# Performance work log

Hardware: AMD Instinct MI355X
Metric: run time of the kernel (lower is better)

The kernel has to match this reference:

```python
import jax, jax.numpy as jnp
import numpy as np

H = 4096        # hidden_size
NH = 32         # heads
HD = H // NH    # head_dim = 128
EPS = 1e-5
MINUS_INF = -10000.0
B, S = 2, 1024


def setup_inputs() -> dict:
    key = jax.random.key(0)
    ks = jax.random.split(key, 7)
    x = jax.random.normal(ks[0], (B, S, H), jnp.float32)
    mask = jnp.zeros((B, 1, 1, S), jnp.float32)  # additive padding mask (0 = keep)
    norm_w = 1.0 + 0.02 * jax.random.normal(ks[1], (H,), jnp.float32)
    norm_b = 0.02 * jax.random.normal(ks[2], (H,), jnp.float32)
    qkv_w = 0.02 * jax.random.normal(ks[3], (H, 3 * H), jnp.float32)
    qkv_b = 0.02 * jax.random.normal(ks[4], (3 * H,), jnp.float32)
    attn_ow = 0.02 * jax.random.normal(ks[5], (H, H), jnp.float32)
    return {"x": x, "mask": mask, "norm_w": norm_w, "norm_b": norm_b,
            "qkv_w": qkv_w, "qkv_b": qkv_b, "attn_ow": attn_ow}


def reference(x, mask, norm_w, norm_b, qkv_w, qkv_b, attn_ow):
    b, s, h = x.shape
    # --- pre-attention layernorm (qkv_gemm fuses this in DeepSpeed) ---
    mu = jnp.mean(x, axis=-1, keepdims=True)
    var = jnp.mean(jnp.square(x - mu), axis=-1, keepdims=True)
    inp_norm = (x - mu) * jax.lax.rsqrt(var + EPS) * norm_w + norm_b
    # --- fused QKV GEMM + bias ---
    qkv = inp_norm @ qkv_w + qkv_b                      # [b, s, 3H]
    q, k, v = jnp.split(qkv, 3, axis=-1)
    q = q.reshape(b, s, NH, HD).transpose(0, 2, 1, 3)   # [b, nh, s, hd]
    k = k.reshape(b, s, NH, HD).transpose(0, 2, 1, 3)
    v = v.reshape(b, s, NH, HD).transpose(0, 2, 1, 3)
    # --- scaled dot-product with triangular (causal) mask + additive input mask ---
    norm_factor = 1.0 / jnp.sqrt(jnp.asarray(HD, x.dtype))
    scores = jnp.einsum('bhqd,bhkd->bhqk', q, k) * norm_factor  # [b, nh, s, s]
    causal = jnp.where(jnp.tril(jnp.ones((s, s), bool)), 0.0, MINUS_INF).astype(x.dtype)
    probs = jax.nn.softmax(scores + causal + mask, axis=-1)
    ctx = jnp.einsum('bhqk,bhkd->bhqd', probs, v)               # [b, nh, s, hd]
    ctx = ctx.transpose(0, 2, 1, 3).reshape(b, s, h)
    # --- output projection (vector_matmul, bias applied later in MLP residual-add) ---
    out = ctx @ attn_ow
    return out
```

## Files before the change

### kernel.cpp

```cpp
#include <hip/hip_runtime.h>
#include <stdint.h>


#define S_LEN 1024
#define HID   4096
#define NHEAD 32
#define HDIM  128

typedef __attribute__((ext_vector_type(8))) short bf16x8;
typedef __attribute__((ext_vector_type(4))) float f32x4;
typedef __attribute__((ext_vector_type(8))) unsigned short us8;

__device__ __forceinline__ unsigned short f2bf(float f) {
    union { float f; unsigned u; } v; v.f = f;
    unsigned r = v.u + 0x7fffu + ((v.u >> 16) & 1u);
    return (unsigned short)(r >> 16);
}

__device__ __forceinline__ void gld16(const unsigned short* g, unsigned short* l) {
    __builtin_amdgcn_global_load_lds(
        (const __attribute__((address_space(1))) void*)g,
        (__attribute__((address_space(3))) void*)l, 16, 0, 0);
}

__global__ __launch_bounds__(256) void ln_kernel(const float* __restrict__ x,
        const float* __restrict__ w, const float* __restrict__ bch,
        unsigned short* __restrict__ out) {
    const int row = blockIdx.x;
    const int t = threadIdx.x;
    const float* xr = x + (size_t)row * HID;
    float4 v[4];
    float sum = 0.f, sq = 0.f;
#pragma unroll
    for (int i = 0; i < 4; i++) {
        v[i] = ((const float4*)xr)[t + (i << 8)];
        sum += v[i].x + v[i].y + v[i].z + v[i].w;
        sq  += v[i].x*v[i].x + v[i].y*v[i].y + v[i].z*v[i].z + v[i].w*v[i].w;
    }
#pragma unroll
    for (int off = 32; off; off >>= 1) {
        sum += __shfl_down(sum, off);
        sq  += __shfl_down(sq, off);
    }
    __shared__ float ssum[4], ssq[4];
    if ((t & 63) == 0) { ssum[t >> 6] = sum; ssq[t >> 6] = sq; }
    __syncthreads();
    const float s_all = ssum[0] + ssum[1] + ssum[2] + ssum[3];
    const float q_all = ssq[0] + ssq[1] + ssq[2] + ssq[3];
    const float mean = s_all * (1.f / HID);
    const float var  = q_all * (1.f / HID) - mean * mean;
    const float rstd = rsqrtf(var + 1e-5f);
    unsigned short* orow = out + (size_t)row * HID;
#pragma unroll
    for (int i = 0; i < 4; i++) {
        float4 wv = ((const float4*)w)[t + (i << 8)];
        float4 bv = ((const float4*)bch)[t + (i << 8)];
        ushort4 o;
        o.x = f2bf((v[i].x - mean) * rstd * wv.x + bv.x);
        o.y = f2bf((v[i].y - mean) * rstd * wv.y + bv.y);
        o.z = f2bf((v[i].z - mean) * rstd * wv.z + bv.z);
        o.w = f2bf((v[i].w - mean) * rstd * wv.w + bv.w);
        ((ushort4*)orow)[t + (i << 8)] = o;
    }
}

__global__ __launch_bounds__(256) void transconv(const float* __restrict__ W,
        unsigned short* __restrict__ Wt, int K, int N) {
    __shared__ float tileT[128 * 65];
    const int n0 = blockIdx.x << 7, k0 = blockIdx.y << 6;
    const int t = threadIdx.x;
#pragma unroll
    for (int it = 0; it < 8; it++) {
        int idx = (it << 8) + t;
        int r = idx >> 5;
        int c4 = idx & 31;
        float4 v = *(const float4*)(W + (size_t)(k0 + r) * N + n0 + (c4 << 2));
        tileT[((c4 << 2) + 0) * 65 + r] = v.x;
        tileT[((c4 << 2) + 1) * 65 + r] = v.y;
        tileT[((c4 << 2) + 2) * 65 + r] = v.z;
        tileT[((c4 << 2) + 3) * 65 + r] = v.w;
    }
    __syncthreads();
#pragma unroll
    for (int it = 0; it < 4; it++) {
        int idx = (it << 8) + t;
        int n = idx >> 3;
        int k8 = idx & 7;
        const float* src = &tileT[n * 65 + (k8 << 3)];
        us8 o;
#pragma unroll
        for (int e = 0; e < 8; e++) o[e] = f2bf(src[e]);
        *(us8*)(Wt + (size_t)(n0 + n) * K + k0 + (k8 << 3)) = o;
    }
}


#define T256_PHASE(CB, KS, IH, READ_B, STAGE_CALL, DO_VM)                         \
  {                                                                               \
    _Pragma("unroll") for (int ii = 0; ii < 4; ii++)                              \
        af[ii] = ldA(CB, KS, ((IH) << 2) + ii);                                   \
    if (READ_B) {                                                                 \
      _Pragma("unroll") for (int jj = 0; jj < 4; jj++) bfv[jj] = ldB(CB, KS, jj); \
    }                                                                             \
    STAGE_CALL;                                                                   \
    __builtin_amdgcn_s_barrier();                                                 \
    asm volatile("s_waitcnt lgkmcnt(0)" ::: "memory");                            \
    __builtin_amdgcn_sched_barrier(0);                                            \
    __builtin_amdgcn_s_setprio(1);                                                \
    _Pragma("unroll") for (int ii = 0; ii < 4; ii++)                              \
      _Pragma("unroll") for (int jj = 0; jj < 4; jj++)                            \
        acc[((IH) << 2) + ii][jj] = __builtin_amdgcn_mfma_f32_16x16x32_bf16(      \
            af[ii], bfv[jj], acc[((IH) << 2) + ii][jj], 0, 0, 0);                 \
    __builtin_amdgcn_s_setprio(0);                                                \
    if (DO_VM) asm volatile("s_waitcnt vmcnt(4)" ::: "memory");                   \
    __builtin_amdgcn_s_barrier();                                                 \
  }

#define T256_TILE(TT, CB, PT)                                                     \
  {                                                                               \
    bf16x8 af[4], bfv[4];                                                         \
    T256_PHASE(CB, 0, 0, 1, stage(GA, (((CB)^1) << 15)        , (PT), 0), 0)      \
    T256_PHASE(CB, 0, 1, 0, stage(GB, (((CB)^1) << 15) + 16384, (PT), 0), 1)      \
    T256_PHASE(CB, 1, 0, 1, stage(GA, (((CB)^1) << 15) +  8192, (PT), 1), 0)      \
    T256_PHASE(CB, 1, 1, 0, stage(GB, (((CB)^1) << 15) + 24576, (PT), 1), 1)      \
  }

__device__ __forceinline__ void gemm_core_256(
        const unsigned short* __restrict__ GA,
        const unsigned short* __restrict__ GB,
        unsigned short* lds,
        f32x4 acc[8][4]) {
    const int t = threadIdx.x;
    const int wave = t >> 6, lane = t & 63, quad = lane >> 4, l16 = lane & 15;
    const int waveM = wave >> 2, waveN = wave & 3;
    const int sq8 = (((lane & 3) ^ ((lane >> 3) & 3)) << 3);

    auto stage = [&](const unsigned short* G, int ldsOff, int tau, int ks) {
#pragma unroll
        for (int u = 0; u < 2; u++) {
            const int grp = (u << 3) + wave;
            const int r = (grp << 4) + (lane >> 2);
            gld16(G + ((size_t)r << 12) + (tau << 6) + (ks << 5) + sq8,
                  lds + ldsOff + (grp << 9));
        }
    };
    auto ldA = [&](int buf, int ks, int i) -> bf16x8 {
        const int r = (waveM << 7) + (i << 4) + l16;
        return ((const bf16x8*)(lds + (buf << 15) + (ks << 13)))
            [(r << 2) + (quad ^ ((r >> 1) & 3))];
    };
    auto ldB = [&](int buf, int ks, int j) -> bf16x8 {
        const int r = (waveN << 6) + (j << 4) + l16;
        return ((const bf16x8*)(lds + (buf << 15) + 16384 + (ks << 13)))
            [(r << 2) + (quad ^ ((r >> 1) & 3))];
    };

    stage(GA, 0,     0, 0);
    stage(GB, 16384, 0, 0);
    stage(GA, 8192,  0, 1);
    stage(GB, 24576, 0, 1);
    asm volatile("s_waitcnt vmcnt(4)" ::: "memory");
    __builtin_amdgcn_s_barrier();

    for (int tt = 0; tt < 64; tt += 2) {
        T256_TILE(tt,     0, tt + 1)
        T256_TILE(tt + 1, 1, (tt == 62) ? 63 : tt + 2)
    }
    asm volatile("s_waitcnt vmcnt(0)" ::: "memory");
}

__global__ __launch_bounds__(512, 2) void gemm_qkv16(
        const unsigned short* __restrict__ A,
        const unsigned short* __restrict__ Bt,
        const float* __restrict__ bias,
        unsigned short* __restrict__ qb,
        unsigned short* __restrict__ kb,
        unsigned short* __restrict__ vt) {
    __shared__ unsigned short lds[65536];
    const int orig = blockIdx.x;
    const int bm = orig & 7, bn = orig >> 3;
    const int t = threadIdx.x;
    const int wave = t >> 6, lane = t & 63, quad = lane >> 4, l16 = lane & 15;
    const int waveM = wave >> 2, waveN = wave & 3;

    const f32x4 fz = {0.f, 0.f, 0.f, 0.f};
    f32x4 acc[8][4];
#pragma unroll
    for (int i = 0; i < 8; i++)
#pragma unroll
        for (int j = 0; j < 4; j++) acc[i][j] = fz;

    gemm_core_256(A + ((size_t)bm << 20), Bt + ((size_t)bn << 20), lds, acc);

    const int nbase = (bn << 8) + (waveN << 6);
    const int which = nbase >> 12;
#pragma unroll
    for (int ii = 0; ii < 8; ii++) {
#pragma unroll
        for (int jj = 0; jj < 4; jj++) {
#pragma unroll
            for (int r = 0; r < 4; r++) {
                int m = (bm << 8) + (waveM << 7) + (ii << 4) + (quad << 2) + r;
                int n = nbase + (jj << 4) + l16;
                float v = acc[ii][jj][r] + bias[n];
                unsigned short bvv = f2bf(v);
                int bb = m >> 10, s = m & 1023;
                int h = n & 4095, head = h >> 7, hd = h & 127;
                size_t bh = (size_t)(bb << 5) + head;
                if (which == 0)      qb[(bh * S_LEN + s) * HDIM + hd] = bvv;
                else if (which == 1) kb[(bh * S_LEN + s) * HDIM + hd] = bvv;
                else                 vt[(bh * HDIM + hd) * S_LEN + s] = bvv;
            }
        }
    }
}


#define GEMM_PHASE(CB, KS, PFT, PFB, DO_VM)                                       \
  {                                                                               \
    bf16x8 af[4], bfv[4];                                                         \
    _Pragma("unroll") for (int ii = 0; ii < 4; ii++) af[ii] = ldA(CB, KS, ii);    \
    _Pragma("unroll") for (int jj = 0; jj < 4; jj++) bfv[jj] = ldB(CB, KS, jj);   \
    stageA(PFT, KS, PFB);                                                         \
    stageB(PFT, KS, PFB);                                                         \
    __builtin_amdgcn_s_barrier();                                                 \
    asm volatile("s_waitcnt lgkmcnt(0)" ::: "memory");                            \
    __builtin_amdgcn_sched_barrier(0);                                            \
    __builtin_amdgcn_s_setprio(1);                                                \
    _Pragma("unroll") for (int ii = 0; ii < 4; ii++)                              \
      _Pragma("unroll") for (int jj = 0; jj < 4; jj++)                            \
        acc[ii][jj] = __builtin_amdgcn_mfma_f32_16x16x32_bf16(                    \
            af[ii], bfv[jj], acc[ii][jj], 0, 0, 0);                               \
    __builtin_amdgcn_s_setprio(0);                                                \
    if (DO_VM) asm volatile("s_waitcnt vmcnt(6)" ::: "memory");                   \
    __builtin_amdgcn_s_barrier();                                                 \
  }

#define GEMM_TILE(TT, CB)                                                         \
  {                                                                               \
    int pf_ = (TT) + 2; if (pf_ > 63) pf_ = 63;                                   \
    GEMM_PHASE(CB, 0, pf_, ((CB) + 2) % 3, 0)                                     \
    GEMM_PHASE(CB, 1, pf_, ((CB) + 2) % 3, 1)                                     \
  }

__device__ __forceinline__ void gemm_core_8w(
        const unsigned short* __restrict__ GA,
        const unsigned short* __restrict__ GB,
        unsigned short* lds,
        f32x4 acc[4][4]) {
    const int t = threadIdx.x;
    const int wave = t >> 6, lane = t & 63, quad = lane >> 4, l16 = lane & 15;
    const int waveM = wave >> 2, waveN = wave & 3;
    const int srow = lane >> 2;
    const int scol = (((lane & 3) ^ ((lane >> 3) & 3)) << 3);

    auto stageA = [&](int tau, int ks, int buf) {
        const int row = (wave << 4) + srow;
        gld16(GA + ((size_t)row << 12) + (tau << 6) + (ks << 5) + scol,
              lds + buf * 24576 + (ks << 12) + (wave << 9));
    };
    auto stageB = [&](int tau, int ks, int buf) {
#pragma unroll
        for (int u = 0; u < 2; u++) {
            const int ii = (wave << 1) + u;
            const int row = (ii << 4) + srow;
            gld16(GB + ((size_t)row << 12) + (tau << 6) + (ks << 5) + scol,
                  lds + buf * 24576 + 8192 + (ks << 13) + (ii << 9));
        }
    };
    auto ldA = [&](int buf, int ks, int ii) -> bf16x8 {
        const int r = (waveM << 6) + (ii << 4) + l16;
        return ((const bf16x8*)(lds + buf * 24576 + (ks << 12)))
            [(r << 2) + (quad ^ ((r >> 1) & 3))];
    };
    auto ldB = [&](int buf, int ks, int jj) -> bf16x8 {
        const int r = (waveN << 6) + (jj << 4) + l16;
        return ((const bf16x8*)(lds + buf * 24576 + 8192 + (ks << 13)))
            [(r << 2) + (quad ^ ((r >> 1) & 3))];
    };

    stageA(0, 0, 0); stageB(0, 0, 0); stageA(0, 1, 0); stageB(0, 1, 0);
    stageA(1, 0, 1); stageB(1, 0, 1); stageA(1, 1, 1); stageB(1, 1, 1);
    asm volatile("s_waitcnt vmcnt(6)" ::: "memory");
    __builtin_amdgcn_s_barrier();

    for (int tb = 0; tb < 63; tb += 3) {
        GEMM_TILE(tb,     0)
        GEMM_TILE(tb + 1, 1)
        GEMM_TILE(tb + 2, 2)
    }
    GEMM_TILE(63, 0)
    asm volatile("s_waitcnt vmcnt(0)" ::: "memory");
}

__global__ __launch_bounds__(512, 2) void gemm_proj8(
        const unsigned short* __restrict__ A,
        const unsigned short* __restrict__ Bt,
        float* __restrict__ outf) {
    __shared__ unsigned short lds[73728];
    const int orig = blockIdx.x;
    const int wg = ((orig & 7) * 32) + (orig >> 3);
    const int bm = wg >> 4, bn = wg & 15;
    const int t = threadIdx.x;
    const int wave = t >> 6, lane = t & 63, quad = lane >> 4, l16 = lane & 15;
    const int waveM = wave >> 2, waveN = wave & 3;

    const f32x4 fz = {0.f, 0.f, 0.f, 0.f};
    f32x4 acc[4][4];
#pragma unroll
    for (int i = 0; i < 4; i++)
#pragma unroll
        for (int j = 0; j < 4; j++) acc[i][j] = fz;

    gemm_core_8w(A + ((size_t)bm << 19), Bt + ((size_t)bn << 20), lds, acc);

#pragma unroll
    for (int ii = 0; ii < 4; ii++)
#pragma unroll
        for (int jj = 0; jj < 4; jj++)
#pragma unroll
            for (int r = 0; r < 4; r++) {
                int m = (bm << 7) + (waveM << 6) + (ii << 4) + (quad << 2) + r;
                int n = (bn << 8) + (waveN << 6) + (jj << 4) + l16;
                outf[((size_t)m << 12) + n] = acc[ii][jj][r];
            }
}

__global__ __launch_bounds__(256) void attn_kernel(
        const unsigned short* __restrict__ qbuf,
        const unsigned short* __restrict__ kbuf,
        const unsigned short* __restrict__ vtbuf,
        const float* __restrict__ mask,
        unsigned short* __restrict__ ctx) {
    __shared__ unsigned short q_lds[64 * 128];
    __shared__ unsigned short k_lds[64 * 128];
    __shared__ unsigned short v_lds[128 * 64];
    __shared__ unsigned short p_lds[64 * 64];
    const int t = threadIdx.x;
    const int wave = t >> 6, lane = t & 63, quad = lane >> 4, l16 = lane & 15;
    const int bq = blockIdx.x, bh = blockIdx.y;
    const int q0 = bq << 6;
    const int b = bh >> 5;
    const unsigned short* Q  = qbuf  + (size_t)bh * S_LEN * HDIM;
    const unsigned short* Kp = kbuf  + (size_t)bh * S_LEN * HDIM;
    const unsigned short* Vp = vtbuf + (size_t)bh * HDIM * S_LEN;

    {
        int r = t >> 4, c = (t & 15) << 3;
#pragma unroll
        for (int it = 0; it < 4; it++)
            gld16(Q + (size_t)(q0 + r + (it << 4)) * HDIM + c,
                  q_lds + ((((it << 8) + (wave << 6))) << 3));
    }

    const f32x4 fz = {0.f, 0.f, 0.f, 0.f};
    f32x4 o[8];
#pragma unroll
    for (int n = 0; n < 8; n++) o[n] = fz;
    float l_i[4] = {0.f, 0.f, 0.f, 0.f};
    const float scale = 0.08838834764831845f;
    const float* mrow = mask + b * S_LEN;

    for (int kt = 0; kt <= bq; kt++) {
        const int k0 = kt << 6;
        {
            int rk = t >> 4, ck = (t & 15) << 3;
            int rv = t >> 3, cv = (t & 7) << 3;
#pragma unroll
            for (int it = 0; it < 4; it++) {
                gld16(Kp + (size_t)(k0 + rk + (it << 4)) * HDIM + ck,
                      k_lds + (((it << 8) + (wave << 6)) << 3));
                gld16(Vp + (size_t)(rv + (it << 5)) * S_LEN + k0 + cv,
                      v_lds + (((it << 8) + (wave << 6)) << 3));
            }
        }
        __syncthreads();

        f32x4 sacc[4];
#pragma unroll
        for (int j = 0; j < 4; j++) sacc[j] = fz;
        const bf16x8* qv = (const bf16x8*)q_lds;
        const bf16x8* kv = (const bf16x8*)k_lds;
#pragma unroll
        for (int kk = 0; kk < 4; kk++) {
            bf16x8 aq = qv[(((wave << 4) + l16) << 4) + (kk << 2) + quad];
#pragma unroll
            for (int j = 0; j < 4; j++) {
                bf16x8 bk = kv[((((j << 4) + l16)) << 4) + (kk << 2) + quad];
                sacc[j] = __builtin_amdgcn_mfma_f32_16x16x32_bf16(aq, bk, sacc[j], 0, 0, 0);
            }
        }

#pragma unroll
        for (int r = 0; r < 4; r++) {
            int qrow = q0 + (wave << 4) + (quad << 2) + r;
#pragma unroll
            for (int j = 0; j < 4; j++) {
                int key = k0 + (j << 4) + l16;
                float x = sacc[j][r] * scale + mrow[key];
                if (key > qrow) x -= 10000.0f;
                float p = __expf(x);
                l_i[r] += p;
                p_lds[((wave << 4) + (quad << 2) + r) * 64 + (j << 4) + l16] = f2bf(p);
            }
        }
        __syncthreads();

        const bf16x8* pvv = (const bf16x8*)p_lds;
        const bf16x8* vv = (const bf16x8*)v_lds;
#pragma unroll
        for (int ks = 0; ks < 2; ks++) {
            bf16x8 ap = pvv[(((wave << 4) + l16) << 3) + (ks << 2) + quad];
#pragma unroll
            for (int n = 0; n < 8; n++) {
                bf16x8 bvv = vv[((((n << 4) + l16)) << 3) + (ks << 2) + quad];
                o[n] = __builtin_amdgcn_mfma_f32_16x16x32_bf16(ap, bvv, o[n], 0, 0, 0);
            }
        }
        __syncthreads();
    }

#pragma unroll
    for (int r = 0; r < 4; r++) {
        float l = l_i[r];
#pragma unroll
        for (int off = 1; off < 16; off <<= 1) l += __shfl_xor(l, off);
        float inv = 1.0f / l;
        int qrow = q0 + (wave << 4) + (quad << 2) + r;
        size_t base = ((size_t)(b * S_LEN + qrow)) * HID + ((size_t)(bh & 31) << 7);
#pragma unroll
        for (int n = 0; n < 8; n++)
            ctx[base + (n << 4) + l16] = f2bf(o[n][r] * inv);
    }
}

extern "C" void kernel_launch(void* const* d_in, const int* in_sizes, int n_in,
                              void* d_out, int out_size, void* d_ws, size_t ws_size,
                              hipStream_t stream) {
    const float* x       = (const float*)d_in[0];
    const float* mask    = (const float*)d_in[1];
    const float* norm_w  = (const float*)d_in[2];
    const float* norm_b  = (const float*)d_in[3];
    const float* qkv_w   = (const float*)d_in[4];
    const float* qkv_b   = (const float*)d_in[5];
    const float* attn_ow = (const float*)d_in[6];
    float* out = (float*)d_out;

    char* ws = (char*)d_ws;
    size_t off = 0;
    auto alloc = [&](size_t bytes) {
        char* p = ws + off;
        off += (bytes + 255) & ~(size_t)255;
        return p;
    };
    unsigned short* inp_norm = (unsigned short*)alloc((size_t)2048 * HID * 2);
    unsigned short* qkv_wt   = (unsigned short*)alloc((size_t)3 * HID * HID * 2);
    unsigned short* ow_t     = (unsigned short*)alloc((size_t)HID * HID * 2);
    unsigned short* qb       = (unsigned short*)alloc((size_t)64 * S_LEN * HDIM * 2);
    unsigned short* kb       = (unsigned short*)alloc((size_t)64 * S_LEN * HDIM * 2);
    unsigned short* vt       = (unsigned short*)alloc((size_t)64 * S_LEN * HDIM * 2);
    unsigned short* ctx      = (unsigned short*)alloc((size_t)2048 * HID * 2);

    ln_kernel<<<2048, 256, 0, stream>>>(x, norm_w, norm_b, inp_norm);
    transconv<<<dim3(3 * HID / 128, HID / 64), 256, 0, stream>>>(qkv_w, qkv_wt, HID, 3 * HID);
    transconv<<<dim3(HID / 128, HID / 64), 256, 0, stream>>>(attn_ow, ow_t, HID, HID);
    gemm_qkv16<<<384, 512, 0, stream>>>(inp_norm, qkv_wt, qkv_b, qb, kb, vt);
    attn_kernel<<<dim3(16, 64), 256, 0, stream>>>(qb, kb, vt, mask, ctx);
    gemm_proj8<<<256, 512, 0, stream>>>(ctx, ow_t, out);
}
```

Before: 810.5 us.

## Retile QKV GEMM to 256x192 blocks for full wave occupancy across CUs

The QKV GEMM moves from 256x256 output tiles (384 blocks) to 256x192 tiles (512 blocks). Each wave now computes 8x3 MFMA tiles, and the B tile is staged once per K-step with a new 8-way swizzle. The goal is to fix wave quantization on the 256-CU part (384 blocks leaves a partial second wave at 2 blocks per CU) and to cut LDS use. The projection GEMM's prefetch staging is also regrouped into its first phase. In exchange, arithmetic intensity per block drops, since the B:A reuse ratio is lower.

```diff
diff --git a/kernel.cpp b/kernel.cpp
--- a/kernel.cpp
+++ b/kernel.cpp
@@ -95,116 +95,117 @@
 }
 
 
-#define T256_PHASE(CB, KS, IH, READ_B, STAGE_CALL, DO_VM)                         \
+#define Q_PHASE(CB, KS, IH, READB, STAGE, VMSTMT)                                 \
   {                                                                               \
     _Pragma("unroll") for (int ii = 0; ii < 4; ii++)                              \
         af[ii] = ldA(CB, KS, ((IH) << 2) + ii);                                   \
-    if (READ_B) {                                                                 \
-      _Pragma("unroll") for (int jj = 0; jj < 4; jj++) bfv[jj] = ldB(CB, KS, jj); \
+    if (READB) {                                                                  \
+      _Pragma("unroll") for (int jj = 0; jj < 3; jj++) bfv[jj] = ldB(CB, KS, jj); \
     }                                                                             \
-    STAGE_CALL;                                                                   \
+    STAGE;                                                                        \
     __builtin_amdgcn_s_barrier();                                                 \
     asm volatile("s_waitcnt lgkmcnt(0)" ::: "memory");                            \
     __builtin_amdgcn_sched_barrier(0);                                            \
     __builtin_amdgcn_s_setprio(1);                                                \
     _Pragma("unroll") for (int ii = 0; ii < 4; ii++)                              \
-      _Pragma("unroll") for (int jj = 0; jj < 4; jj++)                            \
+      _Pragma("unroll") for (int jj = 0; jj < 3; jj++)                            \
         acc[((IH) << 2) + ii][jj] = __builtin_amdgcn_mfma_f32_16x16x32_bf16(      \
             af[ii], bfv[jj], acc[((IH) << 2) + ii][jj], 0, 0, 0);                 \
     __builtin_amdgcn_s_setprio(0);                                                \
-    if (DO_VM) asm volatile("s_waitcnt vmcnt(4)" ::: "memory");                   \
+    VMSTMT;                                                                       \
     __builtin_amdgcn_s_barrier();                                                 \
   }
 
-#define T256_TILE(TT, CB, PT)                                                     \
+#define Q_TILE(TT, CB)                                                            \
   {                                                                               \
-    bf16x8 af[4], bfv[4];                                                         \
-    T256_PHASE(CB, 0, 0, 1, stage(GA, (((CB)^1) << 15)        , (PT), 0), 0)      \
-    T256_PHASE(CB, 0, 1, 0, stage(GB, (((CB)^1) << 15) + 16384, (PT), 0), 1)      \
-    T256_PHASE(CB, 1, 0, 1, stage(GA, (((CB)^1) << 15) +  8192, (PT), 1), 0)      \
-    T256_PHASE(CB, 1, 1, 0, stage(GB, (((CB)^1) << 15) + 24576, (PT), 1), 1)      \
+    bf16x8 af[4], bfv[3];                                                         \
+    int pf_ = (TT) + 1; if (pf_ > 63) pf_ = 63;                                   \
+    Q_PHASE(CB, 0, 0, 1, { stgA(pf_, 0, (CB)^1); stgB(pf_, (CB)^1); }, ((void)0)) \
+    Q_PHASE(CB, 0, 1, 0, ((void)0), asm volatile("s_waitcnt vmcnt(5)":::"memory"))\
+    Q_PHASE(CB, 1, 0, 1, { stgA(pf_, 1, (CB)^1); }, ((void)0))                    \
+    Q_PHASE(CB, 1, 1, 0, ((void)0), asm volatile("s_waitcnt vmcnt(2)":::"memory"))\
   }
 
-__device__ __forceinline__ void gemm_core_256(
-        const unsigned short* __restrict__ GA,
-        const unsigned short* __restrict__ GB,
-        unsigned short* lds,
-        f32x4 acc[8][4]) {
-    const int t = threadIdx.x;
-    const int wave = t >> 6, lane = t & 63, quad = lane >> 4, l16 = lane & 15;
-    const int waveM = wave >> 2, waveN = wave & 3;
-    const int sq8 = (((lane & 3) ^ ((lane >> 3) & 3)) << 3);
-
-    auto stage = [&](const unsigned short* G, int ldsOff, int tau, int ks) {
-#pragma unroll
-        for (int u = 0; u < 2; u++) {
-            const int grp = (u << 3) + wave;
-            const int r = (grp << 4) + (lane >> 2);
-            gld16(G + ((size_t)r << 12) + (tau << 6) + (ks << 5) + sq8,
-                  lds + ldsOff + (grp << 9));
-        }
-    };
-    auto ldA = [&](int buf, int ks, int i) -> bf16x8 {
-        const int r = (waveM << 7) + (i << 4) + l16;
-        return ((const bf16x8*)(lds + (buf << 15) + (ks << 13)))
-            [(r << 2) + (quad ^ ((r >> 1) & 3))];
-    };
-    auto ldB = [&](int buf, int ks, int j) -> bf16x8 {
-        const int r = (waveN << 6) + (j << 4) + l16;
-        return ((const bf16x8*)(lds + (buf << 15) + 16384 + (ks << 13)))
-            [(r << 2) + (quad ^ ((r >> 1) & 3))];
-    };
-
-    stage(GA, 0,     0, 0);
-    stage(GB, 16384, 0, 0);
-    stage(GA, 8192,  0, 1);
-    stage(GB, 24576, 0, 1);
-    asm volatile("s_waitcnt vmcnt(4)" ::: "memory");
-    __builtin_amdgcn_s_barrier();
-
-    for (int tt = 0; tt < 64; tt += 2) {
-        T256_TILE(tt,     0, tt + 1)
-        T256_TILE(tt + 1, 1, (tt == 62) ? 63 : tt + 2)
-    }
-    asm volatile("s_waitcnt vmcnt(0)" ::: "memory");
-}
-
-__global__ __launch_bounds__(512, 2) void gemm_qkv16(
+__global__ __launch_bounds__(512, 2) void gemm_qkv192(
         const unsigned short* __restrict__ A,
         const unsigned short* __restrict__ Bt,
         const float* __restrict__ bias,
         unsigned short* __restrict__ qb,
         unsigned short* __restrict__ kb,
         unsigned short* __restrict__ vt) {
-    __shared__ unsigned short lds[65536];
+    __shared__ unsigned short lds[57344];
     const int orig = blockIdx.x;
     const int bm = orig & 7, bn = orig >> 3;
     const int t = threadIdx.x;
     const int wave = t >> 6, lane = t & 63, quad = lane >> 4, l16 = lane & 15;
     const int waveM = wave >> 2, waveN = wave & 3;
 
+    const unsigned short* GA = A  + ((size_t)bm << 8) * HID;
+    const unsigned short* GB = Bt + ((size_t)bn * 192) * HID;
+
+    const int sqa = (((lane & 3) ^ ((lane >> 3) & 3)) << 3);
+    const int sqb = (((lane & 7) ^ ((lane >> 3) & 7)) << 3);
+
+    auto stgA = [&](int tau, int ks, int buf) {
+#pragma unroll
+        for (int u = 0; u < 2; u++) {
+            const int g = (u << 3) + wave;
+            const int row = (g << 4) + (lane >> 2);
+            gld16(GA + (size_t)row * HID + (tau << 6) + (ks << 5) + sqa,
+                  lds + buf * 28672 + (ks << 13) + (g << 9));
+        }
+    };
+    auto stgB = [&](int tau, int buf) {
+#pragma unroll
+        for (int u = 0; u < 3; u++) {
+            const int g = (u << 3) + wave;
+            const int row = (g << 3) + (lane >> 3);
+            gld16(GB + (size_t)row * HID + (tau << 6) + sqb,
+                  lds + buf * 28672 + 16384 + (g << 9));
+        }
+    };
+    auto ldA = [&](int buf, int ks, int i) -> bf16x8 {
+        const int r = (waveM << 7) + (i << 4) + l16;
+        return ((const bf16x8*)lds)
+            [((buf * 28672 + (ks << 13)) >> 3) + (r << 2) + (quad ^ ((r >> 1) & 3))];
+    };
+    auto ldB = [&](int buf, int ks, int j) -> bf16x8 {
+        const int r = waveN * 48 + (j << 4) + l16;
+        return ((const bf16x8*)lds)
+            [((buf * 28672 + 16384) >> 3) + (r << 3) + (((ks << 2) | quad) ^ (r & 7))];
+    };
+
     const f32x4 fz = {0.f, 0.f, 0.f, 0.f};
-    f32x4 acc[8][4];
+    f32x4 acc[8][3];
 #pragma unroll
     for (int i = 0; i < 8; i++)
 #pragma unroll
-        for (int j = 0; j < 4; j++) acc[i][j] = fz;
-
-    gemm_core_256(A + ((size_t)bm << 20), Bt + ((size_t)bn << 20), lds, acc);
-
-    const int nbase = (bn << 8) + (waveN << 6);
-    const int which = nbase >> 12;
+        for (int j = 0; j < 3; j++) acc[i][j] = fz;
+
+    stgA(0, 0, 0);
+    stgB(0, 0);
+    stgA(0, 1, 0);
+    asm volatile("s_waitcnt vmcnt(2)" ::: "memory");
+    __builtin_amdgcn_s_barrier();
+
+    for (int tt = 0; tt < 64; tt += 2) {
+        Q_TILE(tt,     0)
+        Q_TILE(tt + 1, 1)
+    }
+    asm volatile("s_waitcnt vmcnt(0)" ::: "memory");
+
 #pragma unroll
     for (int ii = 0; ii < 8; ii++) {
 #pragma unroll
-        for (int jj = 0; jj < 4; jj++) {
+        for (int jj = 0; jj < 3; jj++) {
 #pragma unroll
             for (int r = 0; r < 4; r++) {
                 int m = (bm << 8) + (waveM << 7) + (ii << 4) + (quad << 2) + r;
-                int n = nbase + (jj << 4) + l16;
+                int n = bn * 192 + waveN * 48 + (jj << 4) + l16;
                 float v = acc[ii][jj][r] + bias[n];
                 unsigned short bvv = f2bf(v);
                 int bb = m >> 10, s = m & 1023;
+                int which = n >> 12;
                 int h = n & 4095, head = h >> 7, hd = h & 127;
                 size_t bh = (size_t)(bb << 5) + head;
                 if (which == 0)      qb[(bh * S_LEN + s) * HDIM + hd] = bvv;
@@ -216,13 +217,12 @@
 }
 
 
-#define GEMM_PHASE(CB, KS, PFT, PFB, DO_VM)                                       \
+#define GEMM_PHASE(CB, KS, STAGE, VMSTMT)                                         \
   {                                                                               \
     bf16x8 af[4], bfv[4];                                                         \
     _Pragma("unroll") for (int ii = 0; ii < 4; ii++) af[ii] = ldA(CB, KS, ii);    \
     _Pragma("unroll") for (int jj = 0; jj < 4; jj++) bfv[jj] = ldB(CB, KS, jj);   \
-    stageA(PFT, KS, PFB);                                                         \
-    stageB(PFT, KS, PFB);                                                         \
+    STAGE;                                                                        \
     __builtin_amdgcn_s_barrier();                                                 \
     asm volatile("s_waitcnt lgkmcnt(0)" ::: "memory");                            \
     __builtin_amdgcn_sched_barrier(0);                                            \
@@ -232,15 +232,19 @@
         acc[ii][jj] = __builtin_amdgcn_mfma_f32_16x16x32_bf16(                    \
             af[ii], bfv[jj], acc[ii][jj], 0, 0, 0);                               \
     __builtin_amdgcn_s_setprio(0);                                                \
-    if (DO_VM) asm volatile("s_waitcnt vmcnt(6)" ::: "memory");                   \
+    VMSTMT;                                                                       \
     __builtin_amdgcn_s_barrier();                                                 \
   }
 
 #define GEMM_TILE(TT, CB)                                                         \
   {                                                                               \
     int pf_ = (TT) + 2; if (pf_ > 63) pf_ = 63;                                   \
-    GEMM_PHASE(CB, 0, pf_, ((CB) + 2) % 3, 0)                                     \
-    GEMM_PHASE(CB, 1, pf_, ((CB) + 2) % 3, 1)                                     \
+    const int pb_ = ((CB) + 2) % 3;                                               \
+    GEMM_PHASE(CB, 0,                                                             \
+        { stageA(pf_, 0, pb_); stageB(pf_, 0, pb_);                               \
+          stageA(pf_, 1, pb_); stageB(pf_, 1, pb_); }, ((void)0))                 \
+    GEMM_PHASE(CB, 1, ((void)0),                                                  \
+        asm volatile("s_waitcnt vmcnt(6)" ::: "memory"))                          \
   }
 
 __device__ __forceinline__ void gemm_core_8w(
@@ -464,7 +468,7 @@
     ln_kernel<<<2048, 256, 0, stream>>>(x, norm_w, norm_b, inp_norm);
     transconv<<<dim3(3 * HID / 128, HID / 64), 256, 0, stream>>>(qkv_w, qkv_wt, HID, 3 * HID);
     transconv<<<dim3(HID / 128, HID / 64), 256, 0, stream>>>(attn_ow, ow_t, HID, HID);
-    gemm_qkv16<<<384, 512, 0, stream>>>(inp_norm, qkv_wt, qkv_b, qb, kb, vt);
+    gemm_qkv192<<<512, 512, 0, stream>>>(inp_norm, qkv_wt, qkv_b, qb, kb, vt);
     attn_kernel<<<dim3(16, 64), 256, 0, stream>>>(qb, kb, vt, mask, ctx);
     gemm_proj8<<<256, 512, 0, stream>>>(ctx, ow_t, out);
 }
```

Measured after the change: 771.6 us. 1.05x faster.
